# Kernel tuning notes

Measured on AMD Instinct MI355X. Metric: run time of the kernel, lower is better.

Reference implementation:

```python
import jax, jax.numpy as jnp
import numpy as np

N_NODES = 50000
N_EDGES = 800000
IN_CH = 128
HID = 64
NUM_HEADS = 8
NUM_CLASSES = 2
NEG_SLOPE = 0.2   # PyG GATConv default LeakyReLU slope
BN_EPS = 1e-5
SOFTMAX_EPS = 1e-16  # PyG softmax denominator epsilon


def setup_inputs() -> dict:
    key = jax.random.key(0)
    ks = jax.random.split(key, 20)
    s = 0.1
    inp = {
        "x": jax.random.normal(ks[0], (N_NODES, IN_CH), dtype=jnp.float32),
        "edge_index": jax.random.randint(ks[1], (2, N_EDGES), 0, N_NODES, dtype=jnp.int64),
        # layer 0 params, stacked over the 8 independent heads
        "W0": jax.random.normal(ks[2], (NUM_HEADS, IN_CH, HID), dtype=jnp.float32) * s,
        "a_src0": jax.random.normal(ks[3], (NUM_HEADS, HID), dtype=jnp.float32) * s,
        "a_dst0": jax.random.normal(ks[4], (NUM_HEADS, HID), dtype=jnp.float32) * s,
        "b0": jnp.zeros((NUM_HEADS, HID), dtype=jnp.float32),
        "gamma0": jnp.ones((NUM_HEADS, HID), dtype=jnp.float32),
        "beta0": jnp.zeros((NUM_HEADS, HID), dtype=jnp.float32),
        # layer 1 params
        "W1": jax.random.normal(ks[5], (NUM_HEADS, HID, HID), dtype=jnp.float32) * s,
        "a_src1": jax.random.normal(ks[6], (NUM_HEADS, HID), dtype=jnp.float32) * s,
        "a_dst1": jax.random.normal(ks[7], (NUM_HEADS, HID), dtype=jnp.float32) * s,
        "b1": jnp.zeros((NUM_HEADS, HID), dtype=jnp.float32),
        "gamma1": jnp.ones((NUM_HEADS, HID), dtype=jnp.float32),
        "beta1": jnp.zeros((NUM_HEADS, HID), dtype=jnp.float32),
        # ensemble classifier
        "Wc": jax.random.normal(ks[8], (NUM_HEADS * HID, NUM_CLASSES), dtype=jnp.float32) * s,
        "bc": jnp.zeros((NUM_CLASSES,), dtype=jnp.float32),
    }
    return inp


def _gat_layer(x, src, dst, n, W, a_s, a_d, b):
    """Single-head GATConv (PyG semantics, self-loops already in src/dst)."""
    h = x @ W                                           # [N, C]
    logits = (h @ a_s)[src] + (h @ a_d)[dst]            # [E]
    logits = jax.nn.leaky_relu(logits, NEG_SLOPE)
    m = jax.ops.segment_max(logits, dst, num_segments=n)
    ex = jnp.exp(logits - m[dst])
    denom = jax.ops.segment_sum(ex, dst, num_segments=n)
    alpha = ex / (denom[dst] + SOFTMAX_EPS)             # segment softmax over dst
    out = jax.ops.segment_sum(h[src] * alpha[:, None], dst, num_segments=n)
    return out + b


def _bn(h, gamma, beta):
    # BatchNorm1d training-mode math (batch statistics over nodes)
    mu = jnp.mean(h, axis=0)
    var = jnp.var(h, axis=0)
    return (h - mu) * jax.lax.rsqrt(var + BN_EPS) * gamma + beta


def reference(x, edge_index, W0, a_src0, a_dst0, b0, gamma0, beta0,
              W1, a_src1, a_dst1, b1, gamma1, beta1, Wc, bc):
    n = x.shape[0]
    loops = jnp.arange(n, dtype=edge_index.dtype)
    src = jnp.concatenate([edge_index[0], loops])  # PyG add_self_loops=True
    dst = jnp.concatenate([edge_index[1], loops])

    def branch(Wh0, as0, ad0, bh0, g0, be0, Wh1, as1, ad1, bh1, g1, be1):
        h = _gat_layer(x, src, dst, n, Wh0, as0, ad0, bh0)
        h = jax.nn.elu(_bn(h, g0, be0))                  # dropout off (eval)
        h = _gat_layer(h, src, dst, n, Wh1, as1, ad1, bh1)
        h = jax.nn.elu(_bn(h, g1, be1))
        return h                                          # [N, HID]

    hs = jax.vmap(branch)(W0, a_src0, a_dst0, b0, gamma0, beta0,
                          W1, a_src1, a_dst1, b1, gamma1, beta1)  # [H, N, HID]
    feat = jnp.transpose(hs, (1, 0, 2)).reshape(n, -1)            # [N, H*HID]
    return feat @ Wc + bc
```

## Files before the change

### kernel.cpp

```cpp
#include <hip/hip_runtime.h>
#include <hip/hip_bf16.h>
#include <math.h>
#include <stdint.h>

#define N_NODES 50000
#define N_EDGES 800000
#define E_TOT   (N_EDGES + N_NODES)
#define IN_CH   128
#define HID     64
#define NHEAD   8
#define C       512
#define NEG_SLOPE 0.2f
#define BN_EPS    1e-5f
#define SM_EPS    1e-16f
#define SCAN_B    196

typedef __attribute__((ext_vector_type(8))) short bf16x8;
typedef __attribute__((ext_vector_type(4))) float f32x4;

__device__ __forceinline__ float lrelu(float x){ return x > 0.f ? x : NEG_SLOPE * x; }
__device__ __forceinline__ float elu(float x){ return x > 0.f ? x : __expf(x) - 1.f; }
__device__ __forceinline__ float bflo(unsigned u){ return __uint_as_float(u << 16); }
__device__ __forceinline__ float bfhi(unsigned u){ return __uint_as_float(u & 0xffff0000u); }
__device__ __forceinline__ unsigned short f2bf(float f){
  unsigned u = __float_as_uint(f);
  unsigned r = u + 0x7fffu + ((u >> 16) & 1u);
  return (unsigned short)(r >> 16);
}

__global__ void k_detect(const int* __restrict__ ei, int* flag){
  if (threadIdx.x == 0 && blockIdx.x == 0) {
    int f = 1;
    for (int i = 0; i < 32; i++) if (ei[2*i + 1] != 0) f = 0;
    *flag = f;
  }
}
__global__ void k_init_counts(int* counts){
  int i = blockIdx.x * 256 + threadIdx.x;
  if (i < N_NODES) counts[i] = 1;
}
__global__ void k_extract_count(const int* __restrict__ ei, const int* __restrict__ flag,
                                int* __restrict__ src32, int* __restrict__ dst32,
                                int* counts){
  int e = blockIdx.x * 256 + threadIdx.x;
  if (e >= N_EDGES) return;
  int s, d;
  if (*flag) {
    const long long* e64 = (const long long*)ei;
    s = (int)e64[e];
    d = (int)e64[(size_t)N_EDGES + e];
  } else {
    s = ei[e];
    d = ei[N_EDGES + e];
  }
  src32[e] = s; dst32[e] = d;
  atomicAdd(&counts[d], 1);
}

__global__ void k_scan1(const int* __restrict__ counts, int* __restrict__ excl, int* __restrict__ bsum){
  __shared__ int s[256];
  int tid = threadIdx.x;
  int i = blockIdx.x * 256 + tid;
  int v = (i < N_NODES) ? counts[i] : 0;
  s[tid] = v; __syncthreads();
#pragma unroll
  for (int d = 1; d < 256; d <<= 1) {
    int t = (tid >= d) ? s[tid - d] : 0;
    __syncthreads(); s[tid] += t; __syncthreads();
  }
  if (i < N_NODES) excl[i] = s[tid] - v;
  if (tid == 255) bsum[blockIdx.x] = s[255];
}
__global__ void k_scan2(int* bsum){
  __shared__ int s[256];
  int tid = threadIdx.x;
  int v = (tid < SCAN_B) ? bsum[tid] : 0;
  s[tid] = v; __syncthreads();
#pragma unroll
  for (int d = 1; d < 256; d <<= 1) {
    int t = (tid >= d) ? s[tid - d] : 0;
    __syncthreads(); s[tid] += t; __syncthreads();
  }
  if (tid < SCAN_B) bsum[tid] = s[tid] - v;
}
__global__ void k_scan3(const int* __restrict__ excl, const int* __restrict__ bsum,
                        int* __restrict__ off, int* __restrict__ cursor){
  int i = blockIdx.x * 256 + threadIdx.x;
  if (i < N_NODES) { int o = excl[i] + bsum[blockIdx.x]; off[i] = o; cursor[i] = o; }
  if (i == 0) off[N_NODES] = E_TOT;
}
__global__ void k_scatter_self(int* cursor, int* __restrict__ csr_src){
  int i = blockIdx.x * 256 + threadIdx.x;
  if (i < N_NODES) { int p = atomicAdd(&cursor[i], 1); csr_src[p] = i; }
}
__global__ void k_scatter_edges(const int* __restrict__ src, const int* __restrict__ dst,
                                int* cursor, int* __restrict__ csr_src){
  int e = blockIdx.x * 256 + threadIdx.x;
  if (e < N_EDGES) { int d = dst[e]; int p = atomicAdd(&cursor[d], 1); csr_src[p] = src[e]; }
}

__global__ void k_cast_x(const float* __restrict__ X, unsigned short* __restrict__ X16){
  size_t i = (size_t)(blockIdx.x * 256 + threadIdx.x) * 4;
  float4 v = *reinterpret_cast<const float4*>(&X[i]);
  ushort4 p; p.x = f2bf(v.x); p.y = f2bf(v.y); p.z = f2bf(v.z); p.w = f2bf(v.w);
  *reinterpret_cast<ushort4*>(&X16[i]) = p;
}
template<int K>
__global__ void k_transpose_w(const float* __restrict__ W, unsigned short* __restrict__ Bt){
  int i = blockIdx.x * 256 + threadIdx.x;
  int k = i % K; int rem = i / K; int c = rem & 63; int h = rem >> 6;
  Bt[i] = f2bf(W[((size_t)h * K + k) * 64 + c]);
}

__global__ __launch_bounds__(256) void k_gemm0(const unsigned short* __restrict__ X16,
                                               const unsigned short* __restrict__ Bt,
                                               const float* __restrict__ a_src,
                                               const float* __restrict__ a_dst,
                                               unsigned short* __restrict__ H16,
                                               float* __restrict__ s_src,
                                               float* __restrict__ s_dst){
  __shared__ unsigned short LA[64 * 136];
  __shared__ unsigned short LB[64 * 136];
  int r0 = blockIdx.x * 64, h = blockIdx.y;
  int tid = threadIdx.x;
#pragma unroll
  for (int i = 0; i < 4; i++) {
    int idx = tid + i * 256;
    int r = idx >> 4, l16 = idx & 15;
    uint4 v = make_uint4(0, 0, 0, 0);
    if (r0 + r < N_NODES)
      v = *reinterpret_cast<const uint4*>(&X16[(size_t)(r0 + r) * IN_CH + l16 * 8]);
    *reinterpret_cast<uint4*>(&LA[r * 136 + l16 * 8]) = v;
  }
#pragma unroll
  for (int i = 0; i < 4; i++) {
    int idx = tid + i * 256;
    int c = idx >> 4, l16 = idx & 15;
    uint4 v = *reinterpret_cast<const uint4*>(&Bt[(size_t)h * 8192 + c * 128 + l16 * 8]);
    *reinterpret_cast<uint4*>(&LB[c * 136 + l16 * 8]) = v;
  }
  __syncthreads();
  int w = tid >> 6, l = tid & 63;
  int lr = l & 15, lg = l >> 4;
  f32x4 acc[4] = {};
#pragma unroll
  for (int kf = 0; kf < 4; kf++) {
    bf16x8 af = *reinterpret_cast<const bf16x8*>(&LA[(w * 16 + lr) * 136 + kf * 32 + lg * 8]);
#pragma unroll
    for (int cf = 0; cf < 4; cf++) {
      bf16x8 bfr = *reinterpret_cast<const bf16x8*>(&LB[(cf * 16 + lr) * 136 + kf * 32 + lg * 8]);
      acc[cf] = __builtin_amdgcn_mfma_f32_16x16x32_bf16(af, bfr, acc[cf], 0, 0, 0);
    }
  }
#pragma unroll
  for (int cf = 0; cf < 4; cf++)
#pragma unroll
    for (int rr = 0; rr < 4; rr++) {
      int gr = r0 + w * 16 + lg * 4 + rr;
      if (gr < N_NODES)
        H16[(size_t)gr * C + h * HID + cf * 16 + lr] = f2bf(acc[cf][rr]);
    }
  float ps[4] = {}, pd[4] = {};
#pragma unroll
  for (int cf = 0; cf < 4; cf++) {
    float as_ = a_src[h * HID + cf * 16 + lr];
    float ad_ = a_dst[h * HID + cf * 16 + lr];
#pragma unroll
    for (int rr = 0; rr < 4; rr++) { ps[rr] += acc[cf][rr] * as_; pd[rr] += acc[cf][rr] * ad_; }
  }
#pragma unroll
  for (int rr = 0; rr < 4; rr++)
#pragma unroll
    for (int o = 1; o < 16; o <<= 1) { ps[rr] += __shfl_xor(ps[rr], o, 64); pd[rr] += __shfl_xor(pd[rr], o, 64); }
  if (lr == 0) {
#pragma unroll
    for (int rr = 0; rr < 4; rr++) {
      int gr = r0 + w * 16 + lg * 4 + rr;
      if (gr < N_NODES) { s_src[gr * NHEAD + h] = ps[rr]; s_dst[gr * NHEAD + h] = pd[rr]; }
    }
  }
}

__global__ __launch_bounds__(256) void k_gemm1(const float* __restrict__ Hprev,
                                               const unsigned short* __restrict__ Bt,
                                               const float* __restrict__ scale,
                                               const float* __restrict__ shift,
                                               const float* __restrict__ a_src,
                                               const float* __restrict__ a_dst,
                                               unsigned short* __restrict__ H16,
                                               float* __restrict__ s_src,
                                               float* __restrict__ s_dst){
  __shared__ unsigned short LA[64 * 72];
  __shared__ unsigned short LB[64 * 72];
  int r0 = blockIdx.x * 64, h = blockIdx.y;
  int tid = threadIdx.x;
#pragma unroll
  for (int i = 0; i < 4; i++) {
    int idx = tid + i * 256;
    int r = idx >> 4, l16 = idx & 15;
    float4 v = make_float4(0.f, 0.f, 0.f, 0.f);
    if (r0 + r < N_NODES)
      v = *reinterpret_cast<const float4*>(&Hprev[(size_t)(r0 + r) * C + h * HID + l16 * 4]);
    float4 sc = *reinterpret_cast<const float4*>(&scale[h * HID + l16 * 4]);
    float4 sh = *reinterpret_cast<const float4*>(&shift[h * HID + l16 * 4]);
    ushort4 p;
    p.x = f2bf(elu(sc.x * v.x + sh.x));
    p.y = f2bf(elu(sc.y * v.y + sh.y));
    p.z = f2bf(elu(sc.z * v.z + sh.z));
    p.w = f2bf(elu(sc.w * v.w + sh.w));
    *reinterpret_cast<ushort4*>(&LA[r * 72 + l16 * 4]) = p;
  }
#pragma unroll
  for (int i = 0; i < 2; i++) {
    int idx = tid + i * 256;
    int c = idx >> 3, l8 = idx & 7;
    uint4 v = *reinterpret_cast<const uint4*>(&Bt[(size_t)h * 4096 + c * 64 + l8 * 8]);
    *reinterpret_cast<uint4*>(&LB[c * 72 + l8 * 8]) = v;
  }
  __syncthreads();
  int w = tid >> 6, l = tid & 63;
  int lr = l & 15, lg = l >> 4;
  f32x4 acc[4] = {};
#pragma unroll
  for (int kf = 0; kf < 2; kf++) {
    bf16x8 af = *reinterpret_cast<const bf16x8*>(&LA[(w * 16 + lr) * 72 + kf * 32 + lg * 8]);
#pragma unroll
    for (int cf = 0; cf < 4; cf++) {
      bf16x8 bfr = *reinterpret_cast<const bf16x8*>(&LB[(cf * 16 + lr) * 72 + kf * 32 + lg * 8]);
      acc[cf] = __builtin_amdgcn_mfma_f32_16x16x32_bf16(af, bfr, acc[cf], 0, 0, 0);
    }
  }
#pragma unroll
  for (int cf = 0; cf < 4; cf++)
#pragma unroll
    for (int rr = 0; rr < 4; rr++) {
      int gr = r0 + w * 16 + lg * 4 + rr;
      if (gr < N_NODES)
        H16[(size_t)gr * C + h * HID + cf * 16 + lr] = f2bf(acc[cf][rr]);
    }
  float ps[4] = {}, pd[4] = {};
#pragma unroll
  for (int cf = 0; cf < 4; cf++) {
    float as_ = a_src[h * HID + cf * 16 + lr];
    float ad_ = a_dst[h * HID + cf * 16 + lr];
#pragma unroll
    for (int rr = 0; rr < 4; rr++) { ps[rr] += acc[cf][rr] * as_; pd[rr] += acc[cf][rr] * ad_; }
  }
#pragma unroll
  for (int rr = 0; rr < 4; rr++)
#pragma unroll
    for (int o = 1; o < 16; o <<= 1) { ps[rr] += __shfl_xor(ps[rr], o, 64); pd[rr] += __shfl_xor(pd[rr], o, 64); }
  if (lr == 0) {
#pragma unroll
    for (int rr = 0; rr < 4; rr++) {
      int gr = r0 + w * 16 + lg * 4 + rr;
      if (gr < N_NODES) { s_src[gr * NHEAD + h] = ps[rr]; s_dst[gr * NHEAD + h] = pd[rr]; }
    }
  }
}

__global__ __launch_bounds__(256) void k_aggregate(const unsigned short* __restrict__ H16,
                                                   const float* __restrict__ s_src,
                                                   const float* __restrict__ s_dst,
                                                   const int* __restrict__ off,
                                                   const int* __restrict__ csr,
                                                   const float* __restrict__ bias,
                                                   float* __restrict__ Hout){
  __shared__ float alds[4][64][8];
  int wv = threadIdx.x >> 6, lane = threadIdx.x & 63;
  int n = blockIdx.x * 4 + wv;
  if (n >= N_NODES) return;
  int e0 = off[n], deg = off[n + 1] - e0;
  int hsel = lane >> 3;

  float sd[NHEAD];
#pragma unroll
  for (int h = 0; h < NHEAD; h++) sd[h] = s_dst[n * NHEAD + h];

  float acc[8] = {};
  float dnl[NHEAD] = {};

  for (int base = 0; base < deg; base += 64) {
    int e = base + lane;
    int cnt = min(64, deg - base);
    int s_reg = 0;
    if (e < deg) {
      s_reg = csr[e0 + e];
      const float4* sp = reinterpret_cast<const float4*>(&s_src[s_reg * NHEAD]);
      float4 s01 = sp[0], s23 = sp[1];
      float sv[8] = { s01.x, s01.y, s01.z, s01.w, s23.x, s23.y, s23.z, s23.w };
#pragma unroll
      for (int h = 0; h < NHEAD; h++) {
        float ex = __expf(lrelu(sv[h] + sd[h]));
        dnl[h] += ex;
        alds[wv][lane][h] = ex;
      }
    }
#pragma unroll 2
    for (int j = 0; j < cnt; j++) {
      int s = __shfl(s_reg, j, 64);
      float a = alds[wv][j][hsel];
      const uint4* rp = reinterpret_cast<const uint4*>(H16 + (size_t)s * C);
      uint4 v = rp[lane];
      acc[0] += a * bflo(v.x); acc[1] += a * bfhi(v.x);
      acc[2] += a * bflo(v.y); acc[3] += a * bfhi(v.y);
      acc[4] += a * bflo(v.z); acc[5] += a * bfhi(v.z);
      acc[6] += a * bflo(v.w); acc[7] += a * bfhi(v.w);
    }
  }

  float mydn = 0.f;
#pragma unroll
  for (int h = 0; h < NHEAD; h++) {
    float d = dnl[h];
#pragma unroll
    for (int o = 32; o; o >>= 1) d += __shfl_xor(d, o, 64);
    if (hsel == h) mydn = d;
  }
  float inv = 1.f / (mydn + SM_EPS);

  float* op = Hout + (size_t)n * C + lane * 8;
  const float* bp = bias + lane * 8;
  float4 o0, o1;
  o0.x = acc[0]*inv + bp[0]; o0.y = acc[1]*inv + bp[1];
  o0.z = acc[2]*inv + bp[2]; o0.w = acc[3]*inv + bp[3];
  o1.x = acc[4]*inv + bp[4]; o1.y = acc[5]*inv + bp[5];
  o1.z = acc[6]*inv + bp[6]; o1.w = acc[7]*inv + bp[7];
  reinterpret_cast<float4*>(op)[0] = o0;
  reinterpret_cast<float4*>(op)[1] = o1;
}

__global__ void k_zero_stats(float* stats){ stats[threadIdx.x] = 0.f; }
__global__ __launch_bounds__(256) void k_bn_stats(const float* __restrict__ Hm, float* __restrict__ stats){
  int c = threadIdx.x;
  float s0 = 0.f, q0 = 0.f, s1 = 0.f, q1 = 0.f;
  for (int r = blockIdx.x; r < N_NODES; r += gridDim.x) {
    float v0 = Hm[(size_t)r * C + c];
    float v1 = Hm[(size_t)r * C + c + 256];
    s0 += v0; q0 += v0 * v0; s1 += v1; q1 += v1 * v1;
  }
  atomicAdd(&stats[c], s0);
  atomicAdd(&stats[c + 256], s1);
  atomicAdd(&stats[C + c], q0);
  atomicAdd(&stats[C + c + 256], q1);
}
__global__ void k_bn_finalize(const float* __restrict__ stats, const float* __restrict__ gamma,
                              const float* __restrict__ beta, float* __restrict__ scale,
                              float* __restrict__ shift){
  int c = threadIdx.x;
  float mean = stats[c] * (1.f / N_NODES);
  float var  = stats[C + c] * (1.f / N_NODES) - mean * mean;
  float sc = gamma[c] * rsqrtf(var + BN_EPS);
  scale[c] = sc;
  shift[c] = beta[c] - mean * sc;
}

__global__ __launch_bounds__(256) void k_final(const float* __restrict__ Hm,
                                               const float* __restrict__ scale,
                                               const float* __restrict__ shift,
                                               const float* __restrict__ Wc,
                                               const float* __restrict__ bc,
                                               float* __restrict__ out){
  int wave = threadIdx.x >> 6, lane = threadIdx.x & 63;
  int n = blockIdx.x * 4 + wave;
  if (n >= N_NODES) return;
  float a0 = 0.f, a1 = 0.f;
#pragma unroll
  for (int h = 0; h < NHEAD; h++) {
    int ch = h * HID + lane;
    float v = Hm[(size_t)n * C + ch];
    v = scale[ch] * v + shift[ch];
    v = elu(v);
    a0 += v * Wc[ch * 2 + 0];
    a1 += v * Wc[ch * 2 + 1];
  }
#pragma unroll
  for (int o = 32; o; o >>= 1) { a0 += __shfl_xor(a0, o, 64); a1 += __shfl_xor(a1, o, 64); }
  if (lane == 0) { out[n * 2 + 0] = a0 + bc[0]; out[n * 2 + 1] = a1 + bc[1]; }
}

extern "C" void kernel_launch(void* const* d_in, const int* in_sizes, int n_in,
                              void* d_out, int out_size, void* d_ws, size_t ws_size,
                              hipStream_t stream) {
  const float* x      = (const float*)d_in[0];
  const int*   ei     = (const int*)d_in[1];
  const float* W0     = (const float*)d_in[2];
  const float* a_src0 = (const float*)d_in[3];
  const float* a_dst0 = (const float*)d_in[4];
  const float* b0     = (const float*)d_in[5];
  const float* gamma0 = (const float*)d_in[6];
  const float* beta0  = (const float*)d_in[7];
  const float* W1     = (const float*)d_in[8];
  const float* a_src1 = (const float*)d_in[9];
  const float* a_dst1 = (const float*)d_in[10];
  const float* b1     = (const float*)d_in[11];
  const float* gamma1 = (const float*)d_in[12];
  const float* beta1  = (const float*)d_in[13];
  const float* Wc     = (const float*)d_in[14];
  const float* bc     = (const float*)d_in[15];
  float* out = (float*)d_out;

  char* ws = (char*)d_ws;
  size_t o = 0;
  auto alloc = [&](size_t bytes) { char* p = ws + o; o = (o + bytes + 255) & ~(size_t)255; return p; };
  int*   flag    = (int*)  alloc(4);
  int*   src32   = (int*)  alloc((size_t)N_EDGES * 4);
  int*   dst32   = (int*)  alloc((size_t)N_EDGES * 4);
  int*   counts  = (int*)  alloc((size_t)N_NODES * 4);
  int*   excl    = (int*)  alloc((size_t)N_NODES * 4);
  int*   bsum    = (int*)  alloc(256 * 4);
  int*   off     = (int*)  alloc((size_t)(N_NODES + 1) * 4);
  int*   cursor  = (int*)  alloc((size_t)N_NODES * 4);
  int*   csr     = (int*)  alloc((size_t)E_TOT * 4);
  float* s_src   = (float*)alloc((size_t)N_NODES * NHEAD * 4);
  float* s_dst   = (float*)alloc((size_t)N_NODES * NHEAD * 4);
  float* stats   = (float*)alloc(1024 * 4);
  float* scale   = (float*)alloc(C * 4);
  float* shift   = (float*)alloc(C * 4);
  unsigned short* x16  = (unsigned short*)alloc((size_t)N_NODES * IN_CH * 2);
  unsigned short* bt0  = (unsigned short*)alloc((size_t)NHEAD * HID * IN_CH * 2);
  unsigned short* bt1  = (unsigned short*)alloc((size_t)NHEAD * HID * HID * 2);
  unsigned short* h16  = (unsigned short*)alloc((size_t)N_NODES * C * 2);
  float* h_f     = (float*)alloc((size_t)N_NODES * C * 4);

  const int GE = (N_EDGES + 255) / 256;
  const int GN = (N_NODES + 255) / 256;
  const int GW = (N_NODES + 3) / 4;
  const int GR = (N_NODES + 63) / 64;

  k_detect<<<1, 64, 0, stream>>>(ei, flag);
  k_init_counts<<<GN, 256, 0, stream>>>(counts);
  k_extract_count<<<GE, 256, 0, stream>>>(ei, flag, src32, dst32, counts);

  k_cast_x<<<(N_NODES * IN_CH / 4 + 255) / 256, 256, 0, stream>>>(x, x16);
  k_transpose_w<IN_CH><<<(NHEAD * HID * IN_CH + 255) / 256, 256, 0, stream>>>(W0, bt0);
  k_transpose_w<HID><<<(NHEAD * HID * HID + 255) / 256, 256, 0, stream>>>(W1, bt1);

  k_scan1<<<GN, 256, 0, stream>>>(counts, excl, bsum);
  k_scan2<<<1, 256, 0, stream>>>(bsum);
  k_scan3<<<GN, 256, 0, stream>>>(excl, bsum, off, cursor);
  k_scatter_self<<<GN, 256, 0, stream>>>(cursor, csr);
  k_scatter_edges<<<GE, 256, 0, stream>>>(src32, dst32, cursor, csr);

  k_gemm0<<<dim3(GR, NHEAD), 256, 0, stream>>>(x16, bt0, a_src0, a_dst0, h16, s_src, s_dst);
  k_aggregate<<<GW, 256, 0, stream>>>(h16, s_src, s_dst, off, csr, b0, h_f);
  k_zero_stats<<<1, 1024, 0, stream>>>(stats);
  k_bn_stats<<<256, 256, 0, stream>>>(h_f, stats);
  k_bn_finalize<<<1, 512, 0, stream>>>(stats, gamma0, beta0, scale, shift);

  k_gemm1<<<dim3(GR, NHEAD), 256, 0, stream>>>(h_f, bt1, scale, shift, a_src1, a_dst1, h16, s_src, s_dst);
  k_aggregate<<<GW, 256, 0, stream>>>(h16, s_src, s_dst, off, csr, b1, h_f);
  k_zero_stats<<<1, 1024, 0, stream>>>(stats);
  k_bn_stats<<<256, 256, 0, stream>>>(h_f, stats);
  k_bn_finalize<<<1, 512, 0, stream>>>(stats, gamma1, beta1, scale, shift);

  k_final<<<GW, 256, 0, stream>>>(h_f, scale, shift, Wc, bc, out);
}
```

Before: 600.9 us.

## Store aggregated features in bf16 and use per-block partials for BN stats

```diff
diff --git a/kernel.cpp b/kernel.cpp
--- a/kernel.cpp
+++ b/kernel.cpp
@@ -14,6 +14,7 @@
 #define BN_EPS    1e-5f
 #define SM_EPS    1e-16f
 #define SCAN_B    196
+#define STAT_B    256
 
 typedef __attribute__((ext_vector_type(8))) short bf16x8;
 typedef __attribute__((ext_vector_type(4))) float f32x4;
@@ -22,6 +23,7 @@
 __device__ __forceinline__ float elu(float x){ return x > 0.f ? x : __expf(x) - 1.f; }
 __device__ __forceinline__ float bflo(unsigned u){ return __uint_as_float(u << 16); }
 __device__ __forceinline__ float bfhi(unsigned u){ return __uint_as_float(u & 0xffff0000u); }
+__device__ __forceinline__ float bfu(unsigned short u){ return __uint_as_float(((unsigned)u) << 16); }
 __device__ __forceinline__ unsigned short f2bf(float f){
   unsigned u = __float_as_uint(f);
   unsigned r = u + 0x7fffu + ((u >> 16) & 1u);
@@ -84,14 +86,13 @@
   if (tid < SCAN_B) bsum[tid] = s[tid] - v;
 }
 __global__ void k_scan3(const int* __restrict__ excl, const int* __restrict__ bsum,
-                        int* __restrict__ off, int* __restrict__ cursor){
+                        int* __restrict__ off, int* __restrict__ cursor, int* __restrict__ csr){
   int i = blockIdx.x * 256 + threadIdx.x;
-  if (i < N_NODES) { int o = excl[i] + bsum[blockIdx.x]; off[i] = o; cursor[i] = o; }
+  if (i < N_NODES) {
+    int o = excl[i] + bsum[blockIdx.x];
+    off[i] = o; cursor[i] = o + 1; csr[o] = i;
+  }
   if (i == 0) off[N_NODES] = E_TOT;
-}
-__global__ void k_scatter_self(int* cursor, int* __restrict__ csr_src){
-  int i = blockIdx.x * 256 + threadIdx.x;
-  if (i < N_NODES) { int p = atomicAdd(&cursor[i], 1); csr_src[p] = i; }
 }
 __global__ void k_scatter_edges(const int* __restrict__ src, const int* __restrict__ dst,
                                 int* cursor, int* __restrict__ csr_src){
@@ -181,7 +182,7 @@
   }
 }
 
-__global__ __launch_bounds__(256) void k_gemm1(const float* __restrict__ Hprev,
+__global__ __launch_bounds__(256) void k_gemm1(const unsigned short* __restrict__ Hb,
                                                const unsigned short* __restrict__ Bt,
                                                const float* __restrict__ scale,
                                                const float* __restrict__ shift,
@@ -198,16 +199,16 @@
   for (int i = 0; i < 4; i++) {
     int idx = tid + i * 256;
     int r = idx >> 4, l16 = idx & 15;
-    float4 v = make_float4(0.f, 0.f, 0.f, 0.f);
+    ushort4 hv = make_ushort4(0, 0, 0, 0);
     if (r0 + r < N_NODES)
-      v = *reinterpret_cast<const float4*>(&Hprev[(size_t)(r0 + r) * C + h * HID + l16 * 4]);
+      hv = *reinterpret_cast<const ushort4*>(&Hb[(size_t)(r0 + r) * C + h * HID + l16 * 4]);
     float4 sc = *reinterpret_cast<const float4*>(&scale[h * HID + l16 * 4]);
     float4 sh = *reinterpret_cast<const float4*>(&shift[h * HID + l16 * 4]);
     ushort4 p;
-    p.x = f2bf(elu(sc.x * v.x + sh.x));
-    p.y = f2bf(elu(sc.y * v.y + sh.y));
-    p.z = f2bf(elu(sc.z * v.z + sh.z));
-    p.w = f2bf(elu(sc.w * v.w + sh.w));
+    p.x = f2bf(elu(sc.x * bfu(hv.x) + sh.x));
+    p.y = f2bf(elu(sc.y * bfu(hv.y) + sh.y));
+    p.z = f2bf(elu(sc.z * bfu(hv.z) + sh.z));
+    p.w = f2bf(elu(sc.w * bfu(hv.w) + sh.w));
     *reinterpret_cast<ushort4*>(&LA[r * 72 + l16 * 4]) = p;
   }
 #pragma unroll
@@ -265,7 +266,7 @@
                                                    const int* __restrict__ off,
                                                    const int* __restrict__ csr,
                                                    const float* __restrict__ bias,
-                                                   float* __restrict__ Hout){
+                                                   unsigned short* __restrict__ HoutB){
   __shared__ float alds[4][64][8];
   int wv = threadIdx.x >> 6, lane = threadIdx.x & 63;
   int n = blockIdx.x * 4 + wv;
@@ -319,43 +320,59 @@
   }
   float inv = 1.f / (mydn + SM_EPS);
 
-  float* op = Hout + (size_t)n * C + lane * 8;
   const float* bp = bias + lane * 8;
-  float4 o0, o1;
-  o0.x = acc[0]*inv + bp[0]; o0.y = acc[1]*inv + bp[1];
-  o0.z = acc[2]*inv + bp[2]; o0.w = acc[3]*inv + bp[3];
-  o1.x = acc[4]*inv + bp[4]; o1.y = acc[5]*inv + bp[5];
-  o1.z = acc[6]*inv + bp[6]; o1.w = acc[7]*inv + bp[7];
-  reinterpret_cast<float4*>(op)[0] = o0;
-  reinterpret_cast<float4*>(op)[1] = o1;
-}
-
-__global__ void k_zero_stats(float* stats){ stats[threadIdx.x] = 0.f; }
-__global__ __launch_bounds__(256) void k_bn_stats(const float* __restrict__ Hm, float* __restrict__ stats){
-  int c = threadIdx.x;
-  float s0 = 0.f, q0 = 0.f, s1 = 0.f, q1 = 0.f;
-  for (int r = blockIdx.x; r < N_NODES; r += gridDim.x) {
-    float v0 = Hm[(size_t)r * C + c];
-    float v1 = Hm[(size_t)r * C + c + 256];
-    s0 += v0; q0 += v0 * v0; s1 += v1; q1 += v1 * v1;
-  }
-  atomicAdd(&stats[c], s0);
-  atomicAdd(&stats[c + 256], s1);
-  atomicAdd(&stats[C + c], q0);
-  atomicAdd(&stats[C + c + 256], q1);
-}
-__global__ void k_bn_finalize(const float* __restrict__ stats, const float* __restrict__ gamma,
+  ushort4 p0, p1;
+  p0.x = f2bf(acc[0]*inv + bp[0]); p0.y = f2bf(acc[1]*inv + bp[1]);
+  p0.z = f2bf(acc[2]*inv + bp[2]); p0.w = f2bf(acc[3]*inv + bp[3]);
+  p1.x = f2bf(acc[4]*inv + bp[4]); p1.y = f2bf(acc[5]*inv + bp[5]);
+  p1.z = f2bf(acc[6]*inv + bp[6]); p1.w = f2bf(acc[7]*inv + bp[7]);
+  unsigned short* op = HoutB + (size_t)n * C + lane * 8;
+  *reinterpret_cast<ushort4*>(op) = p0;
+  *reinterpret_cast<ushort4*>(op + 4) = p1;
+}
+
+__global__ __launch_bounds__(256) void k_bn_stats(const unsigned short* __restrict__ Hb,
+                                                  float* __restrict__ partial){
+  __shared__ float red[4][64][16];
+  int tid = threadIdx.x, w = tid >> 6, c64 = tid & 63;
+  float s[8] = {}, q[8] = {};
+  for (int r = blockIdx.x * 4 + w; r < N_NODES; r += gridDim.x * 4) {
+    uint4 v = *reinterpret_cast<const uint4*>(&Hb[(size_t)r * C + c64 * 8]);
+    float f[8] = { bflo(v.x), bfhi(v.x), bflo(v.y), bfhi(v.y),
+                   bflo(v.z), bfhi(v.z), bflo(v.w), bfhi(v.w) };
+#pragma unroll
+    for (int k = 0; k < 8; k++) { s[k] += f[k]; q[k] += f[k] * f[k]; }
+  }
+#pragma unroll
+  for (int k = 0; k < 8; k++) { red[w][c64][k] = s[k]; red[w][c64][k + 8] = q[k]; }
+  __syncthreads();
+  if (w == 0) {
+#pragma unroll
+    for (int k = 0; k < 8; k++) {
+      float ss = red[0][c64][k] + red[1][c64][k] + red[2][c64][k] + red[3][c64][k];
+      float qq = red[0][c64][k+8] + red[1][c64][k+8] + red[2][c64][k+8] + red[3][c64][k+8];
+      partial[(size_t)blockIdx.x * 1024 + c64 * 8 + k] = ss;
+      partial[(size_t)blockIdx.x * 1024 + 512 + c64 * 8 + k] = qq;
+    }
+  }
+}
+__global__ void k_bn_finalize(const float* __restrict__ partial, const float* __restrict__ gamma,
                               const float* __restrict__ beta, float* __restrict__ scale,
                               float* __restrict__ shift){
   int c = threadIdx.x;
-  float mean = stats[c] * (1.f / N_NODES);
-  float var  = stats[C + c] * (1.f / N_NODES) - mean * mean;
+  float s = 0.f, q = 0.f;
+  for (int b = 0; b < STAT_B; b++) {
+    s += partial[(size_t)b * 1024 + c];
+    q += partial[(size_t)b * 1024 + 512 + c];
+  }
+  float mean = s * (1.f / N_NODES);
+  float var  = q * (1.f / N_NODES) - mean * mean;
   float sc = gamma[c] * rsqrtf(var + BN_EPS);
   scale[c] = sc;
   shift[c] = beta[c] - mean * sc;
 }
 
-__global__ __launch_bounds__(256) void k_final(const float* __restrict__ Hm,
+__global__ __launch_bounds__(256) void k_final(const unsigned short* __restrict__ Hb,
                                                const float* __restrict__ scale,
                                                const float* __restrict__ shift,
                                                const float* __restrict__ Wc,
@@ -364,15 +381,22 @@
   int wave = threadIdx.x >> 6, lane = threadIdx.x & 63;
   int n = blockIdx.x * 4 + wave;
   if (n >= N_NODES) return;
+  uint4 v = *reinterpret_cast<const uint4*>(&Hb[(size_t)n * C + lane * 8]);
+  float f[8] = { bflo(v.x), bfhi(v.x), bflo(v.y), bfhi(v.y),
+                 bflo(v.z), bfhi(v.z), bflo(v.w), bfhi(v.w) };
+  float4 sc0 = *reinterpret_cast<const float4*>(&scale[lane * 8]);
+  float4 sc1 = *reinterpret_cast<const float4*>(&scale[lane * 8 + 4]);
+  float4 sh0 = *reinterpret_cast<const float4*>(&shift[lane * 8]);
+  float4 sh1 = *reinterpret_cast<const float4*>(&shift[lane * 8 + 4]);
+  float scv[8] = { sc0.x, sc0.y, sc0.z, sc0.w, sc1.x, sc1.y, sc1.z, sc1.w };
+  float shv[8] = { sh0.x, sh0.y, sh0.z, sh0.w, sh1.x, sh1.y, sh1.z, sh1.w };
   float a0 = 0.f, a1 = 0.f;
 #pragma unroll
-  for (int h = 0; h < NHEAD; h++) {
-    int ch = h * HID + lane;
-    float v = Hm[(size_t)n * C + ch];
-    v = scale[ch] * v + shift[ch];
-    v = elu(v);
-    a0 += v * Wc[ch * 2 + 0];
-    a1 += v * Wc[ch * 2 + 1];
+  for (int k = 0; k < 8; k++) {
+    float t = elu(scv[k] * f[k] + shv[k]);
+    int ch = lane * 8 + k;
+    a0 += t * Wc[ch * 2 + 0];
+    a1 += t * Wc[ch * 2 + 1];
   }
 #pragma unroll
   for (int o = 32; o; o >>= 1) { a0 += __shfl_xor(a0, o, 64); a1 += __shfl_xor(a1, o, 64); }
@@ -414,14 +438,14 @@
   int*   csr     = (int*)  alloc((size_t)E_TOT * 4);
   float* s_src   = (float*)alloc((size_t)N_NODES * NHEAD * 4);
   float* s_dst   = (float*)alloc((size_t)N_NODES * NHEAD * 4);
-  float* stats   = (float*)alloc(1024 * 4);
+  float* partial = (float*)alloc((size_t)STAT_B * 1024 * 4);
   float* scale   = (float*)alloc(C * 4);
   float* shift   = (float*)alloc(C * 4);
   unsigned short* x16  = (unsigned short*)alloc((size_t)N_NODES * IN_CH * 2);
   unsigned short* bt0  = (unsigned short*)alloc((size_t)NHEAD * HID * IN_CH * 2);
   unsigned short* bt1  = (unsigned short*)alloc((size_t)NHEAD * HID * HID * 2);
-  unsigned short* h16  = (unsigned short*)alloc((size_t)N_NODES * C * 2);
-  float* h_f     = (float*)alloc((size_t)N_NODES * C * 4);
+  unsigned short* h16a = (unsigned short*)alloc((size_t)N_NODES * C * 2);
+  unsigned short* h16b = (unsigned short*)alloc((size_t)N_NODES * C * 2);
 
   const int GE = (N_EDGES + 255) / 256;
   const int GN = (N_NODES + 255) / 256;
@@ -438,21 +462,18 @@
 
   k_scan1<<<GN, 256, 0, stream>>>(counts, excl, bsum);
   k_scan2<<<1, 256, 0, stream>>>(bsum);
-  k_scan3<<<GN, 256, 0, stream>>>(excl, bsum, off, cursor);
-  k_scatter_self<<<GN, 256, 0, stream>>>(cursor, csr);
+  k_scan3<<<GN, 256, 0, stream>>>(excl, bsum, off, cursor, csr);
   k_scatter_edges<<<GE, 256, 0, stream>>>(src32, dst32, cursor, csr);
 
-  k_gemm0<<<dim3(GR, NHEAD), 256, 0, stream>>>(x16, bt0, a_src0, a_dst0, h16, s_src, s_dst);
-  k_aggregate<<<GW, 256, 0, stream>>>(h16, s_src, s_dst, off, csr, b0, h_f);
-  k_zero_stats<<<1, 1024, 0, stream>>>(stats);
-  k_bn_stats<<<256, 256, 0, stream>>>(h_f, stats);
-  k_bn_finalize<<<1, 512, 0, stream>>>(stats, gamma0, beta0, scale, shift);
-
-  k_gemm1<<<dim3(GR, NHEAD), 256, 0, stream>>>(h_f, bt1, scale, shift, a_src1, a_dst1, h16, s_src, s_dst);
-  k_aggregate<<<GW, 256, 0, stream>>>(h16, s_src, s_dst, off, csr, b1, h_f);
-  k_zero_stats<<<1, 1024, 0, stream>>>(stats);
-  k_bn_stats<<<256, 256, 0, stream>>>(h_f, stats);
-  k_bn_finalize<<<1, 512, 0, stream>>>(stats, gamma1, beta1, scale, shift);
-
-  k_final<<<GW, 256, 0, stream>>>(h_f, scale, shift, Wc, bc, out);
-}
+  k_gemm0<<<dim3(GR, NHEAD), 256, 0, stream>>>(x16, bt0, a_src0, a_dst0, h16a, s_src, s_dst);
+  k_aggregate<<<GW, 256, 0, stream>>>(h16a, s_src, s_dst, off, csr, b0, h16b);
+  k_bn_stats<<<STAT_B, 256, 0, stream>>>(h16b, partial);
+  k_bn_finalize<<<1, 512, 0, stream>>>(partial, gamma0, beta0, scale, shift);
+
+  k_gemm1<<<dim3(GR, NHEAD), 256, 0, stream>>>(h16b, bt1, scale, shift, a_src1, a_dst1, h16a, s_src, s_dst);
+  k_aggregate<<<GW, 256, 0, stream>>>(h16a, s_src, s_dst, off, csr, b1, h16b);
+  k_bn_stats<<<STAT_B, 256, 0, stream>>>(h16b, partial);
+  k_bn_finalize<<<1, 512, 0, stream>>>(partial, gamma1, beta1, scale, shift);
+
+  k_final<<<GW, 256, 0, stream>>>(h16b, scale, shift, Wc, bc, out);
+}
```

Measured after the change: 512.7 us. 1.17x faster.
